# Performance work log

Measured on AMD Instinct MI355X. Metric: run time of the kernel, lower is better.

The kernel has to match this reference:

```python
import jax, jax.numpy as jnp
import numpy as np

# --- basis bookkeeping (mirrors TwoBodyToSpherical._generate_buffers) ---
METADATA = np.array([3, 2, 1], dtype=np.int64)          # shells per l
N_IRREPS = 2 * np.arange(3, dtype=np.int64) + 1          # 2l+1
REP_OFFSETS = np.concatenate([[0], np.cumsum(METADATA * N_IRREPS)[:-1]])
NUM_REPS_1D = int((METADATA * N_IRREPS).sum())           # = 14
M_IDX_MAP = {0: [0], 1: [0, 2, 1], 2: [0, 1, 2, 3, 4]}
ANGULAR = {"s": 0, "p": 1, "d": 2}

C_AOS = ["1s", "2s", "3s"] + ["2p"] * 3 + ["3p"] * 3 + ["3d"] * 5
H_AOS = ["1s", "2s"]


def _build_repid_map(aos):
    # faithful port of the per-element repid_map construction (valence_only=True)
    repid = np.zeros(len(aos), dtype=np.int64)
    dst_n, l_last, m_qc = 0, 0, 0
    for i, ao in enumerate(aos):
        l = ANGULAR[ao[1]]
        if l > l_last:
            dst_n = 0
        repid[i] = REP_OFFSETS[l] + dst_n + M_IDX_MAP[l][m_qc] * METADATA[l]
        if m_qc == 2 * l:
            m_qc = 0
            dst_n += 1
        else:
            m_qc += 1
        l_last = l
    return repid


def setup_inputs() -> dict:
    key = jax.random.key(0)
    maps = {"C": _build_repid_map(C_AOS), "H": _build_repid_map(H_AOS)}
    atomsybs = ["C"] * 400 + ["H"] * 100               # 500 atoms
    n_atoms = len(atomsybs)
    dst_rep_ids_1d = np.concatenate([maps[a] for a in atomsybs])
    lens = np.array([len(maps[a]) for a in atomsybs], dtype=np.int64)
    dst_offsets_1d = np.repeat(np.arange(n_atoms, dtype=np.int64), lens)
    dst_flat_ids_1d = dst_offsets_1d * NUM_REPS_1D + dst_rep_ids_1d  # [N_ao]=5800
    n_ao = dst_flat_ids_1d.shape[0]
    feat_ten = jax.random.normal(key, (n_ao, n_ao), dtype=jnp.float32)
    return {
        "feat_ten": feat_ten,
        "dst_flat_ids_1d": jnp.asarray(dst_flat_ids_1d, dtype=jnp.int32),
        "n_atoms": n_atoms,
        "num_reps_1d": NUM_REPS_1D,
    }


def reference(feat_ten, dst_flat_ids_1d, n_atoms, num_reps_1d):
    total = n_atoms * num_reps_1d                        # 7000
    # 2D destination flat ids: outer-sum of 1D ids (rep_dims=(0,1))
    ids2d = (dst_flat_ids_1d[:, None] * total + dst_flat_ids_1d[None, :]).reshape(-1)
    flat = feat_ten.reshape(-1)
    out_flat = jnp.zeros((total * total,), dtype=feat_ten.dtype).at[ids2d].add(flat)
    # view(n_atoms, R, n_atoms, R) then transpose(1,2) -> [A, A, R, R]
    out = out_flat.reshape(n_atoms, num_reps_1d, n_atoms, num_reps_1d)
    return jnp.transpose(out, (0, 2, 1, 3))
```

## Files before the change

### kernel.cpp

```cpp
#include <hip/hip_runtime.h>

constexpr int R = 14;
constexpr int A = 500;
constexpr int TOTAL = A * R;
constexpr int TILE = R * R;
constexpr int G = 25;
constexpr int NG = A / G;
constexpr int MAXW = G * R;
constexpr int WP = MAXW + 3;
constexpr int CHUNK = G * TILE;

__global__ void init_inv_kernel(int* __restrict__ inv) {
    int t = blockIdx.x * blockDim.x + threadIdx.x;
    if (t < TOTAL) inv[t] = -1;
}

__global__ void build_inv_kernel(const int* __restrict__ dst, int n_ao,
                                 int* __restrict__ inv) {
    int t = blockIdx.x * blockDim.x + threadIdx.x;
    if (t < n_ao) inv[dst[t]] = t;
}

__global__ void atom_info_kernel(const int* __restrict__ inv,
                                 int* __restrict__ arow,
                                 int* __restrict__ ncols,
                                 int* __restrict__ pm) {
    int a = blockIdx.x * blockDim.x + threadIdx.x;
    if (a >= A) return;
    int lo = 0x7fffffff, hi = -1;
#pragma unroll
    for (int r = 0; r < R; ++r) {
        int v = inv[a * R + r];
        if (v >= 0) { lo = min(lo, v); hi = max(hi, v); }
    }
    arow[a] = lo;
    ncols[a] = hi - lo + 1;
#pragma unroll
    for (int r = 0; r < R; ++r) {
        int v = inv[a * R + r];
        pm[a * R + r] = (v >= 0) ? (v - lo) : -1;
    }
}

__global__ __launch_bounds__(256) void tile_kernel(
        const float* __restrict__ feat,
        const int* __restrict__ arow,
        const int* __restrict__ ncols,
        const int* __restrict__ pm,
        float* __restrict__ out, int n_ao) {
    const int g  = blockIdx.x % NG;
    const int a1 = blockIdx.x / NG;
    const int g0 = g * G;
    const int tid = threadIdx.x;

    __shared__ float buf[R][WP];
    __shared__ int s_pr[R];
    __shared__ int s_pc[G * R];
    __shared__ int s_off[G];

    const int arow1 = arow[a1];
    const int n1    = ncols[a1];
    const int colL  = arow[g0];
    const int W     = arow[g0 + G - 1] + ncols[g0 + G - 1] - colL;

    for (int t = tid; t < G * R; t += 256) s_pc[t] = pm[g0 * R + t];
    if (tid < R) s_pr[tid] = pm[a1 * R + tid];
    if (tid < G) s_off[tid] = arow[g0 + tid] - colL;

    for (int d = 0; d < n1; ++d) {
        const float* src = feat + (long long)(arow1 + d) * n_ao + colL;
        for (int c = tid; c < W; c += 256) buf[d][c] = src[c];
    }
    __syncthreads();

    const long long outbase = ((long long)a1 * A + g0) * (long long)TILE;
    for (int o4 = tid * 4; o4 < CHUNK; o4 += 1024) {
        float4 v;
        float* vp = &v.x;
#pragma unroll
        for (int k = 0; k < 4; ++k) {
            int o   = o4 + k;
            int a2i = o / TILE;
            int e   = o - a2i * TILE;
            int r1  = e / R;
            int r2  = e - r1 * R;
            int d   = s_pr[r1];
            int c   = s_pc[a2i * R + r2];
            float val = 0.0f;
            if ((d | c) >= 0) val = buf[d][s_off[a2i] + c];
            vp[k] = val;
        }
        *reinterpret_cast<float4*>(out + outbase + o4) = v;
    }
}

extern "C" void kernel_launch(void* const* d_in, const int* in_sizes, int n_in,
                              void* d_out, int out_size, void* d_ws, size_t ws_size,
                              hipStream_t stream) {
    const float* feat = (const float*)d_in[0];
    const int*   dst  = (const int*)d_in[1];
    int n_ao = in_sizes[1];

    int* inv   = (int*)d_ws;
    int* arow  = inv + TOTAL;
    int* ncols = arow + A;
    int* pm    = ncols + A;

    init_inv_kernel<<<(TOTAL + 255) / 256, 256, 0, stream>>>(inv);
    build_inv_kernel<<<(n_ao + 255) / 256, 256, 0, stream>>>(dst, n_ao, inv);
    atom_info_kernel<<<(A + 255) / 256, 256, 0, stream>>>(inv, arow, ncols, pm);

    tile_kernel<<<A * NG, 256, 0, stream>>>(feat, arow, ncols, pm,
                                            (float*)d_out, n_ao);
}
```

Baseline: 356.6 us.

## Fuse setup kernels, vectorize row loads, and loop super-groups per block

Merges the three index-setup kernels into one single-block kernel to cut launch overhead. The tile kernel now uses 512 threads and processes four column groups per block in a loop, which cuts the block count by a factor of four. It loads source rows with aligned float4 reads into a padded shared buffer and computes indices incrementally for each float4 output. The single-block setup serializes that work, and the per-iteration syncs may limit how well loads and stores overlap.

```diff
diff --git a/kernel.cpp b/kernel.cpp
--- a/kernel.cpp
+++ b/kernel.cpp
@@ -6,51 +6,46 @@
 constexpr int TILE = R * R;
 constexpr int G = 25;
 constexpr int NG = A / G;
+constexpr int SUPER = 4;
+constexpr int NSUP = NG / SUPER;
 constexpr int MAXW = G * R;
-constexpr int WP = MAXW + 3;
+constexpr int WP = 360;
 constexpr int CHUNK = G * TILE;
 
-__global__ void init_inv_kernel(int* __restrict__ inv) {
-    int t = blockIdx.x * blockDim.x + threadIdx.x;
-    if (t < TOTAL) inv[t] = -1;
-}
-
-__global__ void build_inv_kernel(const int* __restrict__ dst, int n_ao,
-                                 int* __restrict__ inv) {
-    int t = blockIdx.x * blockDim.x + threadIdx.x;
-    if (t < n_ao) inv[dst[t]] = t;
-}
-
-__global__ void atom_info_kernel(const int* __restrict__ inv,
-                                 int* __restrict__ arow,
-                                 int* __restrict__ ncols,
-                                 int* __restrict__ pm) {
-    int a = blockIdx.x * blockDim.x + threadIdx.x;
-    if (a >= A) return;
-    int lo = 0x7fffffff, hi = -1;
+__global__ __launch_bounds__(1024) void setup_kernel(
+        const int* __restrict__ dst, int n_ao,
+        int* __restrict__ inv, int* __restrict__ arow,
+        int* __restrict__ ncols, int* __restrict__ pm) {
+    int tid = threadIdx.x;
+    for (int t = tid; t < TOTAL; t += 1024) inv[t] = -1;
+    __syncthreads();
+    for (int t = tid; t < n_ao; t += 1024) inv[dst[t]] = t;
+    __syncthreads();
+    if (tid < A) {
+        int a = tid, lo = 0x7fffffff, hi = -1;
 #pragma unroll
-    for (int r = 0; r < R; ++r) {
-        int v = inv[a * R + r];
-        if (v >= 0) { lo = min(lo, v); hi = max(hi, v); }
-    }
-    arow[a] = lo;
-    ncols[a] = hi - lo + 1;
+        for (int r = 0; r < R; ++r) {
+            int v = inv[a * R + r];
+            if (v >= 0) { lo = min(lo, v); hi = max(hi, v); }
+        }
+        arow[a] = lo;
+        ncols[a] = hi - lo + 1;
 #pragma unroll
-    for (int r = 0; r < R; ++r) {
-        int v = inv[a * R + r];
-        pm[a * R + r] = (v >= 0) ? (v - lo) : -1;
+        for (int r = 0; r < R; ++r) {
+            int v = inv[a * R + r];
+            pm[a * R + r] = (v >= 0) ? (v - lo) : -1;
+        }
     }
 }
 
-__global__ __launch_bounds__(256) void tile_kernel(
+__global__ __launch_bounds__(512) void tile_kernel(
         const float* __restrict__ feat,
         const int* __restrict__ arow,
         const int* __restrict__ ncols,
         const int* __restrict__ pm,
         float* __restrict__ out, int n_ao) {
-    const int g  = blockIdx.x % NG;
-    const int a1 = blockIdx.x / NG;
-    const int g0 = g * G;
+    const int gs  = blockIdx.x % NSUP;
+    const int a1  = blockIdx.x / NSUP;
     const int tid = threadIdx.x;
 
     __shared__ float buf[R][WP];
@@ -60,37 +55,50 @@
 
     const int arow1 = arow[a1];
     const int n1    = ncols[a1];
-    const int colL  = arow[g0];
-    const int W     = arow[g0 + G - 1] + ncols[g0 + G - 1] - colL;
+    if (tid < R) s_pr[tid] = pm[a1 * R + tid];
 
-    for (int t = tid; t < G * R; t += 256) s_pc[t] = pm[g0 * R + t];
-    if (tid < R) s_pr[tid] = pm[a1 * R + tid];
-    if (tid < G) s_off[tid] = arow[g0 + tid] - colL;
+    const int d0 = tid >> 7;
+    const int c4 = tid & 127;
 
-    for (int d = 0; d < n1; ++d) {
-        const float* src = feat + (long long)(arow1 + d) * n_ao + colL;
-        for (int c = tid; c < W; c += 256) buf[d][c] = src[c];
-    }
-    __syncthreads();
+    for (int s = 0; s < SUPER; ++s) {
+        const int g0   = (gs * SUPER + s) * G;
+        const int colL = arow[g0];
+        const int colA = colL & ~3;
+        const int colR = arow[g0 + G - 1] + ncols[g0 + G - 1];
+        const int W4   = (colR - colA + 3) >> 2;
 
-    const long long outbase = ((long long)a1 * A + g0) * (long long)TILE;
-    for (int o4 = tid * 4; o4 < CHUNK; o4 += 1024) {
-        float4 v;
-        float* vp = &v.x;
-#pragma unroll
-        for (int k = 0; k < 4; ++k) {
-            int o   = o4 + k;
-            int a2i = o / TILE;
-            int e   = o - a2i * TILE;
+        for (int t = tid; t < G * R; t += 512) s_pc[t] = pm[g0 * R + t];
+        if (tid < G) s_off[tid] = arow[g0 + tid] - colA;
+
+        if (c4 < W4) {
+            const float4* src4 =
+                (const float4*)(feat + (long long)arow1 * n_ao + colA);
+            const int rs4 = n_ao >> 2;
+            for (int d = d0; d < n1; d += 4)
+                *(float4*)&buf[d][c4 << 2] = src4[(long long)d * rs4 + c4];
+        }
+        __syncthreads();
+
+        const long long outbase = ((long long)a1 * A + g0) * (long long)TILE;
+        for (int o4 = tid * 4; o4 < CHUNK; o4 += 2048) {
+            int a2i = o4 / TILE;
+            int e   = o4 - a2i * TILE;
             int r1  = e / R;
             int r2  = e - r1 * R;
             int d   = s_pr[r1];
-            int c   = s_pc[a2i * R + r2];
-            float val = 0.0f;
-            if ((d | c) >= 0) val = buf[d][s_off[a2i] + c];
-            vp[k] = val;
+            int off = s_off[a2i];
+            const int* pc = &s_pc[a2i * R];
+            float4 v;
+            float* vp = &v.x;
+#pragma unroll
+            for (int k = 0; k < 4; ++k) {
+                int c = pc[r2];
+                vp[k] = ((d | c) >= 0) ? buf[d][off + c] : 0.0f;
+                if (++r2 == R) { r2 = 0; d = s_pr[++r1]; }
+            }
+            *reinterpret_cast<float4*>(out + outbase + o4) = v;
         }
-        *reinterpret_cast<float4*>(out + outbase + o4) = v;
+        __syncthreads();
     }
 }
 
@@ -106,10 +114,7 @@
     int* ncols = arow + A;
     int* pm    = ncols + A;
 
-    init_inv_kernel<<<(TOTAL + 255) / 256, 256, 0, stream>>>(inv);
-    build_inv_kernel<<<(n_ao + 255) / 256, 256, 0, stream>>>(dst, n_ao, inv);
-    atom_info_kernel<<<(A + 255) / 256, 256, 0, stream>>>(inv, arow, ncols, pm);
-
-    tile_kernel<<<A * NG, 256, 0, stream>>>(feat, arow, ncols, pm,
-                                            (float*)d_out, n_ao);
+    setup_kernel<<<1, 1024, 0, stream>>>(dst, n_ao, inv, arow, ncols, pm);
+    tile_kernel<<<A * NSUP, 512, 0, stream>>>(feat, arow, ncols, pm,
+                                              (float*)d_out, n_ao);
 }
```

Result: faster. 317.3 us (-11.0%).
